# Kernel optimization log

Hardware: AMD Instinct MI355X
Metric: run time of the kernel (lower is better)

Reference implementation:

```python
import jax, jax.numpy as jnp
import numpy as np

ITERATIONS = 3

def setup_inputs() -> dict:
    key = jax.random.key(0)
    k1, k2 = jax.random.split(key)
    C, S, H = 64, 128, 2048
    x = jax.random.normal(k1, (C, S, H), dtype=jnp.float32)
    W = jax.random.normal(k2, (H, H), dtype=jnp.float32)
    return {"x": x, "W": W}

def reference(x, W):
    # x: [C, S, H], W: [H, H]
    C, S, H = x.shape
    # e_ij is loop-invariant in the original; hoist it (same math, computed once)
    e_ij = jnp.einsum('csh,hk->csk', x, W)  # [C, S, H]
    b_ij = jnp.zeros((C, S), dtype=x.dtype)
    c_i = jnp.zeros((C, H), dtype=x.dtype)
    for _ in range(ITERATIONS):
        d_i = jax.nn.softmax(b_ij, axis=1)[:, :, None]          # [C, S, 1], softmax over S
        c_i = jnp.sum(d_i * e_ij, axis=1)                        # [C, H]
        squared = jnp.sum(c_i ** 2, axis=1, keepdims=True)       # [C, 1]
        coeff = squared / (1.0 + squared) / jnp.sqrt(squared + 1e-9)
        c_i = coeff * c_i                                        # squash
        b_ij = b_ij + jnp.einsum('csh,ch->cs', e_ij, c_i)        # logit update
    return c_i
```

## Files before the change

kernel.cpp:

```cpp
#include <hip/hip_runtime.h>

using bf16x8 = __attribute__((ext_vector_type(8))) __bf16;
using f32x4  = __attribute__((ext_vector_type(4))) float;

#define C_ 64
#define S_ 128
#define H_ 2048
#define M_ 8192

__device__ __forceinline__ unsigned short f2bf(float f) {
  unsigned u = __float_as_uint(f);
  u = u + 0x7fffu + ((u >> 16) & 1u);
  return (unsigned short)(u >> 16);
}
__device__ __forceinline__ float bf2f(unsigned short h) {
  return __uint_as_float(((unsigned)h) << 16);
}

__device__ __forceinline__ void glds16(const unsigned short* g, unsigned short* l) {
  __builtin_amdgcn_global_load_lds(
      (const __attribute__((address_space(1))) void*)g,
      (__attribute__((address_space(3))) void*)l, 16, 0, 0);
}

__global__ void k_split_x(const float* __restrict__ x,
                          unsigned short* __restrict__ xh,
                          unsigned short* __restrict__ xl) {
  int idx = blockIdx.x * 256 + threadIdx.x;
  float4 v = ((const float4*)x)[idx];
  float a[4] = {v.x, v.y, v.z, v.w};
  unsigned short h[4], l[4];
#pragma unroll
  for (int q = 0; q < 4; ++q) {
    h[q] = f2bf(a[q]);
    l[q] = f2bf(a[q] - bf2f(h[q]));
  }
  ((ushort4*)xh)[idx] = make_ushort4(h[0], h[1], h[2], h[3]);
  ((ushort4*)xl)[idx] = make_ushort4(l[0], l[1], l[2], l[3]);
}

__global__ void k_split_tw(const float* __restrict__ W,
                           unsigned short* __restrict__ Wth,
                           unsigned short* __restrict__ Wtl) {
  __shared__ float Ts[64][68];
  const int t = threadIdx.x;
  const int k0 = blockIdx.x * 64, n0 = blockIdx.y * 64;
#pragma unroll
  for (int p = 0; p < 4; ++p) {
    int idx = t + p * 256;
    int r = idx >> 4, c4 = (idx & 15) * 4;
    *(float4*)&Ts[r][c4] = *(const float4*)(W + (size_t)(k0 + r) * H_ + n0 + c4);
  }
  __syncthreads();
#pragma unroll
  for (int p = 0; p < 4; ++p) {
    int idx = t + p * 256;
    int rr = idx >> 4, cc = (idx & 15) * 4;
    unsigned short h[4], l[4];
#pragma unroll
    for (int q = 0; q < 4; ++q) {
      float f = Ts[cc + q][rr];
      h[q] = f2bf(f);
      l[q] = f2bf(f - bf2f(h[q]));
    }
    size_t o = (size_t)(n0 + rr) * H_ + k0 + cc;
    *(ushort4*)(Wth + o) = make_ushort4(h[0], h[1], h[2], h[3]);
    *(ushort4*)(Wtl + o) = make_ushort4(l[0], l[1], l[2], l[3]);
  }
}

__global__ __launch_bounds__(256, 4) void k_gemm3(
    const unsigned short* __restrict__ Ah, const unsigned short* __restrict__ Al,
    const unsigned short* __restrict__ Bh, const unsigned short* __restrict__ Bl,
    unsigned short* __restrict__ Eh, unsigned short* __restrict__ El) {
  __shared__ unsigned short sAh[128 * 32], sAl[128 * 32], sBh[128 * 32], sBl[128 * 32];
  const int t = threadIdx.x;
  const int bn = blockIdx.x, bm = blockIdx.y;
  const int lane = t & 63, wid = t >> 6;
  const int wm = wid >> 1, wn = wid & 1;
  const int l16 = lane & 15, quad = lane >> 4;

  const int rl = lane >> 2;
  const int gg = (lane & 3) ^ ((rl >> 1) & 3);
  const int c0 = wid * 2, c1 = wid * 2 + 1;
  const unsigned short* gAh0 = Ah + (size_t)(bm * 128 + c0 * 16 + rl) * H_ + gg * 8;
  const unsigned short* gAh1 = Ah + (size_t)(bm * 128 + c1 * 16 + rl) * H_ + gg * 8;
  const unsigned short* gAl0 = Al + (size_t)(bm * 128 + c0 * 16 + rl) * H_ + gg * 8;
  const unsigned short* gAl1 = Al + (size_t)(bm * 128 + c1 * 16 + rl) * H_ + gg * 8;
  const unsigned short* gBh0 = Bh + (size_t)(bn * 128 + c0 * 16 + rl) * H_ + gg * 8;
  const unsigned short* gBh1 = Bh + (size_t)(bn * 128 + c1 * 16 + rl) * H_ + gg * 8;
  const unsigned short* gBl0 = Bl + (size_t)(bn * 128 + c0 * 16 + rl) * H_ + gg * 8;
  const unsigned short* gBl1 = Bl + (size_t)(bn * 128 + c1 * 16 + rl) * H_ + gg * 8;
  unsigned short* lA0 = sAh + c0 * 512;
  unsigned short* lA1 = sAh + c1 * 512;
  unsigned short* lAl0 = sAl + c0 * 512;
  unsigned short* lAl1 = sAl + c1 * 512;
  unsigned short* lB0 = sBh + c0 * 512;
  unsigned short* lB1 = sBh + c1 * 512;
  unsigned short* lBl0 = sBl + c0 * 512;
  unsigned short* lBl1 = sBl + c1 * 512;

  const int swz = ((l16 >> 1) & 3);
  const int colq = ((quad ^ swz) * 8);

  f32x4 acc[4][4];
#pragma unroll
  for (int i = 0; i < 4; ++i)
#pragma unroll
    for (int j = 0; j < 4; ++j) acc[i][j] = (f32x4)0.f;

  for (int k0 = 0; k0 < H_; k0 += 32) {
    __syncthreads();
    glds16(gAh0 + k0, lA0);
    glds16(gAh1 + k0, lA1);
    glds16(gAl0 + k0, lAl0);
    glds16(gAl1 + k0, lAl1);
    glds16(gBh0 + k0, lB0);
    glds16(gBh1 + k0, lB1);
    glds16(gBl0 + k0, lBl0);
    glds16(gBl1 + k0, lBl1);
    __syncthreads();

    bf16x8 ah[4], al[4], bh[4], bl[4];
#pragma unroll
    for (int i = 0; i < 4; ++i) {
      const int ra = (wm * 64 + i * 16 + l16) * 32;
      const int rb = (wn * 64 + i * 16 + l16) * 32;
      ah[i] = *(const bf16x8*)&sAh[ra + colq];
      al[i] = *(const bf16x8*)&sAl[ra + colq];
      bh[i] = *(const bf16x8*)&sBh[rb + colq];
      bl[i] = *(const bf16x8*)&sBl[rb + colq];
    }
#pragma unroll
    for (int i = 0; i < 4; ++i)
#pragma unroll
      for (int j = 0; j < 4; ++j) {
        acc[i][j] = __builtin_amdgcn_mfma_f32_16x16x32_bf16(ah[i], bh[j], acc[i][j], 0, 0, 0);
        acc[i][j] = __builtin_amdgcn_mfma_f32_16x16x32_bf16(ah[i], bl[j], acc[i][j], 0, 0, 0);
        acc[i][j] = __builtin_amdgcn_mfma_f32_16x16x32_bf16(al[i], bh[j], acc[i][j], 0, 0, 0);
      }
  }

#pragma unroll
  for (int i = 0; i < 4; ++i) {
    const int row0 = bm * 128 + wm * 64 + i * 16 + quad * 4;
#pragma unroll
    for (int j = 0; j < 4; ++j) {
      const int col = bn * 128 + wn * 64 + j * 16 + l16;
#pragma unroll
      for (int r = 0; r < 4; ++r) {
        float v = acc[i][j][r];
        unsigned short hh = f2bf(v);
        unsigned short ll = f2bf(v - bf2f(hh));
        Eh[(size_t)(row0 + r) * H_ + col] = hh;
        El[(size_t)(row0 + r) * H_ + col] = ll;
      }
    }
  }
}

__global__ __launch_bounds__(256, 4) void k_gram_mfma(
    const unsigned short* __restrict__ Eh, const unsigned short* __restrict__ El,
    float* __restrict__ G) {
  __shared__ unsigned short sH[128 * 32], sL[128 * 32];
  const int t = threadIdx.x;
  const int kc = blockIdx.x;
  const int cc = blockIdx.y;
  const int lane = t & 63, wid = t >> 6;
  const int wm = wid >> 1, wn = wid & 1;
  const int l16 = lane & 15, quad = lane >> 4;

  const int rl = lane >> 2;
  const int gg = (lane & 3) ^ ((rl >> 1) & 3);
  const int c0 = wid * 2, c1 = c0 + 1;
  const size_t kbase = (size_t)kc * 256 + gg * 8;
  const unsigned short* gH0 = Eh + (size_t)(cc * 128 + c0 * 16 + rl) * H_ + kbase;
  const unsigned short* gH1 = Eh + (size_t)(cc * 128 + c1 * 16 + rl) * H_ + kbase;
  const unsigned short* gL0 = El + (size_t)(cc * 128 + c0 * 16 + rl) * H_ + kbase;
  const unsigned short* gL1 = El + (size_t)(cc * 128 + c1 * 16 + rl) * H_ + kbase;
  unsigned short* lH0 = sH + c0 * 512;
  unsigned short* lH1 = sH + c1 * 512;
  unsigned short* lL0 = sL + c0 * 512;
  unsigned short* lL1 = sL + c1 * 512;

  const int swz = ((l16 >> 1) & 3);
  const int colq = ((quad ^ swz) * 8);

  f32x4 acc[4][4];
#pragma unroll
  for (int i = 0; i < 4; ++i)
#pragma unroll
    for (int j = 0; j < 4; ++j) acc[i][j] = (f32x4)0.f;

  for (int k0 = 0; k0 < 256; k0 += 32) {
    __syncthreads();
    glds16(gH0 + k0, lH0);
    glds16(gH1 + k0, lH1);
    glds16(gL0 + k0, lL0);
    glds16(gL1 + k0, lL1);
    __syncthreads();

    bf16x8 ah[4], al[4], bh[4], bl[4];
#pragma unroll
    for (int i = 0; i < 4; ++i) {
      const int ra = (wm * 64 + i * 16 + l16) * 32;
      const int rb = (wn * 64 + i * 16 + l16) * 32;
      ah[i] = *(const bf16x8*)&sH[ra + colq];
      al[i] = *(const bf16x8*)&sL[ra + colq];
      bh[i] = *(const bf16x8*)&sH[rb + colq];
      bl[i] = *(const bf16x8*)&sL[rb + colq];
    }
#pragma unroll
    for (int i = 0; i < 4; ++i)
#pragma unroll
      for (int j = 0; j < 4; ++j) {
        acc[i][j] = __builtin_amdgcn_mfma_f32_16x16x32_bf16(ah[i], bh[j], acc[i][j], 0, 0, 0);
        acc[i][j] = __builtin_amdgcn_mfma_f32_16x16x32_bf16(ah[i], bl[j], acc[i][j], 0, 0, 0);
        acc[i][j] = __builtin_amdgcn_mfma_f32_16x16x32_bf16(al[i], bh[j], acc[i][j], 0, 0, 0);
      }
  }

  float* Gc = G + (size_t)cc * S_ * S_;
#pragma unroll
  for (int i = 0; i < 4; ++i) {
    const int row0 = wm * 64 + i * 16 + quad * 4;
#pragma unroll
    for (int j = 0; j < 4; ++j) {
      const int col = wn * 64 + j * 16 + l16;
#pragma unroll
      for (int r = 0; r < 4; ++r)
        atomicAdd(&Gc[(row0 + r) * S_ + col], acc[i][j][r]);
    }
  }
}

__global__ void k_iter(const float* __restrict__ G, float* __restrict__ wv) {
  const int c = blockIdx.x;
  const int s = threadIdx.x;
  __shared__ float dsh[128];
  __shared__ float red[128];
  const float* Gc = G + (size_t)c * S_ * S_;
  float b = 0.f;
  for (int it = 0; it < 3; ++it) {
    red[s] = b; __syncthreads();
    for (int off = 64; off > 0; off >>= 1) {
      if (s < off) red[s] = fmaxf(red[s], red[s + off]);
      __syncthreads();
    }
    float mx = red[0]; __syncthreads();
    float ev = expf(b - mx);
    red[s] = ev; __syncthreads();
    for (int off = 64; off > 0; off >>= 1) {
      if (s < off) red[s] = red[s] + red[s + off];
      __syncthreads();
    }
    float Z = red[0]; __syncthreads();
    float d = ev / Z;
    dsh[s] = d; __syncthreads();
    float y = 0.f;
#pragma unroll 8
    for (int j = 0; j < S_; ++j) y = fmaf(Gc[j * S_ + s], dsh[j], y);
    red[s] = d * y; __syncthreads();
    for (int off = 64; off > 0; off >>= 1) {
      if (s < off) red[s] = red[s] + red[s + off];
      __syncthreads();
    }
    float sq = red[0]; __syncthreads();
    float coeff = sq / (1.f + sq) / sqrtf(sq + 1e-9f);
    if (it == 2) wv[c * S_ + s] = coeff * d;
    else b += coeff * y;
  }
}

__global__ void k_out(const unsigned short* __restrict__ Eh,
                      const unsigned short* __restrict__ El,
                      const float* __restrict__ wv, float* __restrict__ out) {
  const int c = blockIdx.y;
  const int h = blockIdx.x * 256 + threadIdx.x;
  __shared__ float wsh[128];
  if (threadIdx.x < 128) wsh[threadIdx.x] = wv[c * S_ + threadIdx.x];
  __syncthreads();
  const unsigned short* Ph = Eh + (size_t)c * S_ * H_ + h;
  const unsigned short* Pl = El + (size_t)c * S_ * H_ + h;
  float acc = 0.f;
#pragma unroll 8
  for (int s = 0; s < S_; ++s)
    acc = fmaf(wsh[s], bf2f(Ph[(size_t)s * H_]) + bf2f(Pl[(size_t)s * H_]), acc);
  out[(size_t)c * H_ + h] = acc;
}

extern "C" void kernel_launch(void* const* d_in, const int* in_sizes, int n_in,
                              void* d_out, int out_size, void* d_ws, size_t ws_size,
                              hipStream_t stream) {
  (void)in_sizes; (void)n_in; (void)out_size; (void)ws_size;
  const float* x = (const float*)d_in[0];
  const float* W = (const float*)d_in[1];
  float* out = (float*)d_out;
  char* ws = (char*)d_ws;

  unsigned short* xh  = (unsigned short*)(ws);
  unsigned short* xl  = (unsigned short*)(ws + 33554432);
  unsigned short* Wth = (unsigned short*)(ws + 67108864);
  unsigned short* Wtl = (unsigned short*)(ws + 75497472);
  unsigned short* Eh  = (unsigned short*)(ws + 83886080);
  unsigned short* El  = (unsigned short*)(ws + 117440512);
  float*          G   = (float*)(ws + 150994944);
  float*          wv  = (float*)(ws + 155189248);

  hipMemsetAsync(G, 0, (size_t)C_ * S_ * S_ * sizeof(float), stream);
  k_split_x<<<dim3(16384), 256, 0, stream>>>(x, xh, xl);
  k_split_tw<<<dim3(32, 32), 256, 0, stream>>>(W, Wth, Wtl);
  k_gemm3<<<dim3(16, 64), 256, 0, stream>>>(xh, xl, Wth, Wtl, Eh, El);
  k_gram_mfma<<<dim3(8, 64), 256, 0, stream>>>(Eh, El, G);
  k_iter<<<dim3(64), 128, 0, stream>>>(G, wv);
  k_out<<<dim3(8, 64), 256, 0, stream>>>(Eh, El, wv, out);
}
```

Before: 383.8 us.

## Fuse split kernels with G zeroing and fuse routing iterations into output kernel

The x split, the W transpose-split and the zeroing of G (previously a memset) are merged into one launch that picks its role from the block index. The routing-iteration kernel is merged into the output kernel: each output block recomputes the softmax and squash iterations for its capsule in shared memory, then reads packed pairs of bf16 values to produce two outputs per thread. This removes several launches and the global round trip for the weight vector, at the cost of recomputing the iterations redundantly in four blocks per capsule. The 256-thread blocks map two threads onto each position in the iteration phase, which makes benign duplicate writes to shared memory.

```diff
diff --git a/kernel.cpp b/kernel.cpp
--- a/kernel.cpp
+++ b/kernel.cpp
@@ -23,49 +23,56 @@
       (__attribute__((address_space(3))) void*)l, 16, 0, 0);
 }
 
-__global__ void k_split_x(const float* __restrict__ x,
-                          unsigned short* __restrict__ xh,
-                          unsigned short* __restrict__ xl) {
-  int idx = blockIdx.x * 256 + threadIdx.x;
-  float4 v = ((const float4*)x)[idx];
-  float a[4] = {v.x, v.y, v.z, v.w};
-  unsigned short h[4], l[4];
-#pragma unroll
-  for (int q = 0; q < 4; ++q) {
-    h[q] = f2bf(a[q]);
-    l[q] = f2bf(a[q] - bf2f(h[q]));
-  }
-  ((ushort4*)xh)[idx] = make_ushort4(h[0], h[1], h[2], h[3]);
-  ((ushort4*)xl)[idx] = make_ushort4(l[0], l[1], l[2], l[3]);
-}
-
-__global__ void k_split_tw(const float* __restrict__ W,
-                           unsigned short* __restrict__ Wth,
-                           unsigned short* __restrict__ Wtl) {
+__global__ void k_split_all(const float* __restrict__ x,
+                            unsigned short* __restrict__ xh,
+                            unsigned short* __restrict__ xl,
+                            const float* __restrict__ W,
+                            unsigned short* __restrict__ Wth,
+                            unsigned short* __restrict__ Wtl,
+                            float* __restrict__ G) {
   __shared__ float Ts[64][68];
+  const int b = blockIdx.x;
   const int t = threadIdx.x;
-  const int k0 = blockIdx.x * 64, n0 = blockIdx.y * 64;
-#pragma unroll
-  for (int p = 0; p < 4; ++p) {
-    int idx = t + p * 256;
-    int r = idx >> 4, c4 = (idx & 15) * 4;
-    *(float4*)&Ts[r][c4] = *(const float4*)(W + (size_t)(k0 + r) * H_ + n0 + c4);
-  }
-  __syncthreads();
-#pragma unroll
-  for (int p = 0; p < 4; ++p) {
-    int idx = t + p * 256;
-    int rr = idx >> 4, cc = (idx & 15) * 4;
+  if (b < 16384) {
+    int idx = b * 256 + t;
+    float4 v = ((const float4*)x)[idx];
+    float a[4] = {v.x, v.y, v.z, v.w};
     unsigned short h[4], l[4];
 #pragma unroll
     for (int q = 0; q < 4; ++q) {
-      float f = Ts[cc + q][rr];
-      h[q] = f2bf(f);
-      l[q] = f2bf(f - bf2f(h[q]));
-    }
-    size_t o = (size_t)(n0 + rr) * H_ + k0 + cc;
-    *(ushort4*)(Wth + o) = make_ushort4(h[0], h[1], h[2], h[3]);
-    *(ushort4*)(Wtl + o) = make_ushort4(l[0], l[1], l[2], l[3]);
+      h[q] = f2bf(a[q]);
+      l[q] = f2bf(a[q] - bf2f(h[q]));
+    }
+    ((ushort4*)xh)[idx] = make_ushort4(h[0], h[1], h[2], h[3]);
+    ((ushort4*)xl)[idx] = make_ushort4(l[0], l[1], l[2], l[3]);
+  } else if (b < 17408) {
+    const int bb = b - 16384;
+    const int k0 = (bb & 31) * 64, n0 = (bb >> 5) * 64;
+#pragma unroll
+    for (int p = 0; p < 4; ++p) {
+      int idx = t + p * 256;
+      int r = idx >> 4, c4 = (idx & 15) * 4;
+      *(float4*)&Ts[r][c4] = *(const float4*)(W + (size_t)(k0 + r) * H_ + n0 + c4);
+    }
+    __syncthreads();
+#pragma unroll
+    for (int p = 0; p < 4; ++p) {
+      int idx = t + p * 256;
+      int rr = idx >> 4, cc = (idx & 15) * 4;
+      unsigned short h[4], l[4];
+#pragma unroll
+      for (int q = 0; q < 4; ++q) {
+        float f = Ts[cc + q][rr];
+        h[q] = f2bf(f);
+        l[q] = f2bf(f - bf2f(h[q]));
+      }
+      size_t o = (size_t)(n0 + rr) * H_ + k0 + cc;
+      *(ushort4*)(Wth + o) = make_ushort4(h[0], h[1], h[2], h[3]);
+      *(ushort4*)(Wtl + o) = make_ushort4(l[0], l[1], l[2], l[3]);
+    }
+  } else {
+    const int bb = b - 17408;
+    ((float4*)G)[bb * 256 + t] = (float4){0.f, 0.f, 0.f, 0.f};
   }
 }
 
@@ -234,11 +241,14 @@
   }
 }
 
-__global__ void k_iter(const float* __restrict__ G, float* __restrict__ wv) {
-  const int c = blockIdx.x;
-  const int s = threadIdx.x;
+__global__ void k_out2(const unsigned short* __restrict__ Eh,
+                       const unsigned short* __restrict__ El,
+                       const float* __restrict__ G, float* __restrict__ out) {
+  const int c = blockIdx.y;
+  const int s = threadIdx.x & 127;
   __shared__ float dsh[128];
   __shared__ float red[128];
+  __shared__ float wsh[128];
   const float* Gc = G + (size_t)c * S_ * S_;
   float b = 0.f;
   for (int it = 0; it < 3; ++it) {
@@ -267,26 +277,23 @@
     }
     float sq = red[0]; __syncthreads();
     float coeff = sq / (1.f + sq) / sqrtf(sq + 1e-9f);
-    if (it == 2) wv[c * S_ + s] = coeff * d;
+    if (it == 2) wsh[s] = coeff * d;
     else b += coeff * y;
   }
-}
-
-__global__ void k_out(const unsigned short* __restrict__ Eh,
-                      const unsigned short* __restrict__ El,
-                      const float* __restrict__ wv, float* __restrict__ out) {
-  const int c = blockIdx.y;
-  const int h = blockIdx.x * 256 + threadIdx.x;
-  __shared__ float wsh[128];
-  if (threadIdx.x < 128) wsh[threadIdx.x] = wv[c * S_ + threadIdx.x];
   __syncthreads();
-  const unsigned short* Ph = Eh + (size_t)c * S_ * H_ + h;
-  const unsigned short* Pl = El + (size_t)c * S_ * H_ + h;
-  float acc = 0.f;
+
+  const int h2 = blockIdx.x * 256 + threadIdx.x;
+  const unsigned* Ph = (const unsigned*)(Eh + (size_t)c * S_ * H_) + h2;
+  const unsigned* Pl = (const unsigned*)(El + (size_t)c * S_ * H_) + h2;
+  float a0 = 0.f, a1 = 0.f;
 #pragma unroll 8
-  for (int s = 0; s < S_; ++s)
-    acc = fmaf(wsh[s], bf2f(Ph[(size_t)s * H_]) + bf2f(Pl[(size_t)s * H_]), acc);
-  out[(size_t)c * H_ + h] = acc;
+  for (int ss = 0; ss < S_; ++ss) {
+    unsigned uh = Ph[(size_t)ss * (H_ / 2)];
+    unsigned ul = Pl[(size_t)ss * (H_ / 2)];
+    a0 = fmaf(wsh[ss], bf2f((unsigned short)uh) + bf2f((unsigned short)ul), a0);
+    a1 = fmaf(wsh[ss], bf2f((unsigned short)(uh >> 16)) + bf2f((unsigned short)(ul >> 16)), a1);
+  }
+  ((float2*)(out + (size_t)c * H_))[h2] = make_float2(a0, a1);
 }
 
 extern "C" void kernel_launch(void* const* d_in, const int* in_sizes, int n_in,
@@ -305,13 +312,9 @@
   unsigned short* Eh  = (unsigned short*)(ws + 83886080);
   unsigned short* El  = (unsigned short*)(ws + 117440512);
   float*          G   = (float*)(ws + 150994944);
-  float*          wv  = (float*)(ws + 155189248);
-
-  hipMemsetAsync(G, 0, (size_t)C_ * S_ * S_ * sizeof(float), stream);
-  k_split_x<<<dim3(16384), 256, 0, stream>>>(x, xh, xl);
-  k_split_tw<<<dim3(32, 32), 256, 0, stream>>>(W, Wth, Wtl);
+
+  k_split_all<<<dim3(18432), 256, 0, stream>>>(x, xh, xl, W, Wth, Wtl, G);
   k_gemm3<<<dim3(16, 64), 256, 0, stream>>>(xh, xl, Wth, Wtl, Eh, El);
   k_gram_mfma<<<dim3(8, 64), 256, 0, stream>>>(Eh, El, G);
-  k_iter<<<dim3(64), 128, 0, stream>>>(G, wv);
-  k_out<<<dim3(8, 64), 256, 0, stream>>>(Eh, El, wv, out);
-}
+  k_out2<<<dim3(4, 64), 256, 0, stream>>>(Eh, El, G, out);
+}
```

Measured after the change: 380.5 us. About the same (-0.9%).
